# Kernel tuning notes

Measured on AMD Instinct MI355X. Metric: run time of the kernel, lower is better.

## Reference

```python
import jax, jax.numpy as jnp
import numpy as np

B, S, N_CATE, N_CONT = 32, 1024, 4, 4
HIDDEN, ATTN, VOCAB, EMB = 1024, 512, 1000, 128


def sinusoidal_pe(seq_len, d_model, base=10000.0):
    pos = jnp.arange(seq_len, dtype=jnp.float32)[:, None]            # [S,1]
    i = jnp.arange(d_model // 2, dtype=jnp.float32)[None, :]         # [1,D/2]
    ang = pos / jnp.power(base, 2.0 * i / d_model)                   # [S,D/2]
    pe = jnp.zeros((seq_len, d_model), dtype=jnp.float32)
    pe = pe.at[:, 0::2].set(jnp.sin(ang))
    pe = pe.at[:, 1::2].set(jnp.cos(ang))
    return pe


def setup_inputs() -> dict:
    key = jax.random.key(0)
    ks = jax.random.split(key, 20)
    s = 0.02
    inp = {
        "cate_x": jax.random.randint(ks[0], (B, S, N_CATE), 0, VOCAB, dtype=jnp.int64)
                  if jax.config.read("jax_enable_x64") else
                  jax.random.randint(ks[0], (B, S, N_CATE), 0, VOCAB, dtype=jnp.int32),
        "cont_x": jax.random.normal(ks[1], (B, S, N_CONT), dtype=jnp.float32),
        "mask": jnp.ones((B, S), dtype=bool),
        "targets": jax.random.uniform(ks[2], (B, S), dtype=jnp.float32),
        # EntireEmbedding params: 4 cate tables + cont linear + comb projection
        "E0": jax.random.normal(ks[3], (VOCAB, EMB), dtype=jnp.float32) * s,
        "E1": jax.random.normal(ks[4], (VOCAB, EMB), dtype=jnp.float32) * s,
        "E2": jax.random.normal(ks[5], (VOCAB, EMB), dtype=jnp.float32) * s,
        "E3": jax.random.normal(ks[6], (VOCAB, EMB), dtype=jnp.float32) * s,
        "Wc": jax.random.normal(ks[7], (N_CONT, N_CATE * EMB), dtype=jnp.float32) * s,
        "Wproj": jax.random.normal(ks[8], (2 * N_CATE * EMB, HIDDEN), dtype=jnp.float32) * s,
        # two-head attention linears (bias=False)
        "WQ1": jax.random.normal(ks[9], (HIDDEN, ATTN), dtype=jnp.float32) * s,
        "WK1": jax.random.normal(ks[10], (HIDDEN, ATTN), dtype=jnp.float32) * s,
        "WV1": jax.random.normal(ks[11], (HIDDEN, ATTN), dtype=jnp.float32) * s,
        "WQ2": jax.random.normal(ks[12], (HIDDEN, ATTN), dtype=jnp.float32) * s,
        "WK2": jax.random.normal(ks[13], (HIDDEN, ATTN), dtype=jnp.float32) * s,
        "WV2": jax.random.normal(ks[14], (HIDDEN, ATTN), dtype=jnp.float32) * s,
        "W0": jax.random.normal(ks[15], (2 * ATTN, HIDDEN), dtype=jnp.float32) * s,
        "Wf": jax.random.normal(ks[16], (HIDDEN, 1), dtype=jnp.float32) * s,
    }
    return inp


def _attend(x, WQ, WK, WV):
    Q = x @ WQ  # [B,S,A]
    K = x @ WK
    V = x @ WV
    scores = jnp.einsum("bqd,bkd->bqk", Q, K) / jnp.sqrt(jnp.float32(ATTN))
    # faithful to nn.Softmax(dim=1): normalize over the QUERY axis
    attn = jax.nn.softmax(scores, axis=1)
    return jnp.einsum("bqk,bkv->bqv", attn, V)


def reference(cate_x, cont_x, mask, targets, E0, E1, E2, E3, Wc, Wproj,
              WQ1, WK1, WV1, WQ2, WK2, WV2, W0, Wf):
    # EntireEmbedding: per-feature cate embeddings + cont projection -> comb proj
    cate_emb = jnp.concatenate(
        [E0[cate_x[..., 0]], E1[cate_x[..., 1]], E2[cate_x[..., 2]], E3[cate_x[..., 3]]],
        axis=-1)                                   # [B,S,512]
    cont_emb = cont_x @ Wc                          # [B,S,512]
    x = jnp.concatenate([cate_emb, cont_emb], axis=-1) @ Wproj  # [B,S,H]
    x = x + sinusoidal_pe(x.shape[1], HIDDEN)[None, :, :]
    z1 = _attend(x, WQ1, WK1, WV1)                  # [B,S,A]
    z2 = _attend(x, WQ2, WK2, WV2)                  # [B,S,A]
    z = jnp.concatenate([z1, z2], axis=-1) @ W0     # [B,S,H]
    out = jax.nn.sigmoid(z @ Wf)                    # FinalConnecting: Linear(H,1)+sigmoid
    return out.squeeze(-1)                          # [B,S]
```

## Files before the change

### kernel.cpp

```cpp
#include <hip/hip_runtime.h>
#include <hip/hip_bf16.h>
#include <math.h>

#define BB    32
#define SS    1024
#define HID   1024
#define AT    512
#define NVOC  1000
#define NT    (BB*SS)

typedef unsigned short u16;
typedef __attribute__((ext_vector_type(8))) short s16x8;
typedef __attribute__((ext_vector_type(4))) float f32x4;

__device__ __forceinline__ float bf2f(u16 u) {
    union { unsigned int i; float f; } x; x.i = ((unsigned int)u) << 16; return x.f;
}
__device__ __forceinline__ u16 f2bf(float f) {
    union { float f; unsigned int i; } u; u.f = f;
    unsigned int r = u.i + 0x7fffu + ((u.i >> 16) & 1u);
    return (u16)(r >> 16);
}
__device__ __forceinline__ float4 ld4(const float* p) { return *(const float4*)p; }
__device__ __forceinline__ float4 ld4bf(const u16* p) {
    ushort4 v = *(const ushort4*)p;
    return make_float4(bf2f(v.x), bf2f(v.y), bf2f(v.z), bf2f(v.w));
}

__device__ __forceinline__ void gld16(const u16* g, u16* l) {
    __builtin_amdgcn_global_load_lds(
        (const __attribute__((address_space(1))) unsigned int*)g,
        (__attribute__((address_space(3))) unsigned int*)l,
        16, 0, 0);
}

struct Ptrs4f { const float* p[4]; };

__device__ __forceinline__ float blockReduceSum(float x) {
    #pragma unroll
    for (int off = 32; off > 0; off >>= 1) x += __shfl_down(x, off, 64);
    __shared__ float tmp[4];
    int lane = threadIdx.x & 63, wid = threadIdx.x >> 6;
    if (lane == 0) tmp[wid] = x;
    __syncthreads();
    if (threadIdx.x == 0) x = tmp[0] + tmp[1] + tmp[2] + tmp[3];
    return x;
}
__device__ __forceinline__ float waveReduceSum(float x) {
    #pragma unroll
    for (int off = 32; off > 0; off >>= 1) x += __shfl_down(x, off, 64);
    return x;
}

__global__ void k_prep(Ptrs4f E, const float* __restrict__ Wproj,
                       u16* __restrict__ PE16, u16* __restrict__ E16o, u16* __restrict__ Wp16) {
    int blk = blockIdx.x, tid = threadIdx.x;
    if (blk < 2048) {
        int idx = blk*256 + tid;
        int s = idx >> 9, i = idx & 511;
        const float l2_10000 = 13.287712379549449f;
        float denom = exp2f((2.f * (float)i / 1024.f) * l2_10000);
        float ang = (float)s / denom;
        unsigned int pack = ((unsigned int)f2bf(cosf(ang)) << 16) | f2bf(sinf(ang));
        *(unsigned int*)(PE16 + (size_t)s*1024 + 2*i) = pack;
    } else if (blk < 4048) {
        int id2 = blk - 2048;
        int f = id2 / 500;
        int i = (id2 % 500)*256 + tid;
        E16o[(size_t)f*128000 + i] = f2bf(E.p[f][i]);
    } else {
        int i = (blk - 4048)*256 + tid;
        Wp16[i] = f2bf(Wproj[i]);
    }
}

__global__ void k_transp(Ptrs4f src, u16* __restrict__ dst, int R, int C) {
    const float* in = src.p[blockIdx.z];
    u16* out = dst + (size_t)blockIdx.z * R * C;
    int r0 = blockIdx.y*32, c0 = blockIdx.x*32;
    __shared__ float tt[32][33];
    tt[threadIdx.y][threadIdx.x] = in[(size_t)(r0 + threadIdx.y)*C + c0 + threadIdx.x];
    __syncthreads();
    out[(size_t)(c0 + threadIdx.y)*R + r0 + threadIdx.x] = f2bf(tt[threadIdx.x][threadIdx.y]);
}

__global__ void k_pre1(const float* __restrict__ W0, const float* __restrict__ Wf,
                       const float* __restrict__ Wc, const float* __restrict__ Wproj,
                       float* __restrict__ W0f, float* __restrict__ Wcp, float* __restrict__ CQ) {
    int blk = blockIdx.x, tid = threadIdx.x;
    if (blk < 1024) {
        const float* row = W0 + (size_t)blk*1024;
        float a = 0.f;
        for (int j = tid; j < 1024; j += 256) a += row[j] * Wf[j];
        a = blockReduceSum(a);
        if (tid == 0) W0f[blk] = a;
    } else if (blk < 1040) {
        int r = blk - 1024; int c = r >> 2, is = r & 3; int i = is*256 + tid;
        float a = 0.f;
        for (int j = 0; j < 512; ++j) a += Wc[c*512 + j] * Wproj[(size_t)(512 + j)*1024 + i];
        Wcp[c*1024 + i] = a;
    } else {
        int r = blk - 1040;
        CQ[r*256 + tid] = 0.f;
    }
}

__global__ void k_pre2(Ptrs4f W, const float* __restrict__ WV1, const float* __restrict__ WV2,
                       const float* __restrict__ W0f, const float* __restrict__ Wcp,
                       float* __restrict__ v, float* __restrict__ CQ) {
    int blk = blockIdx.x, tid = threadIdx.x;
    if (blk < 2048) {
        int h = blk >> 10, i = blk & 1023;
        const float* WV = h ? WV2 : WV1;
        const float* wf = W0f + h*512;
        float a = 0.f;
        for (int aa = tid; aa < 512; aa += 256) a += WV[(size_t)i*512 + aa] * wf[aa];
        a = blockReduceSum(a);
        if (tid == 0) v[h*1024 + i] = a;
    } else {
        int r = blk - 2048;
        int ns = r & 1, wc = (r >> 1) & 15, jc = r >> 5;
        int w = wc & 3, c = wc >> 2; int n = ns*256 + tid;
        const float* Ww = W.p[w];
        float a = 0.f;
        for (int j = jc*128; j < jc*128 + 128; ++j) a += Wcp[c*1024 + j] * Ww[(size_t)j*512 + n];
        atomicAdd(&CQ[(size_t)(w*4 + c)*512 + n], a);
    }
}

__device__ __forceinline__ void cstore(float* p, float v) { *p = v; }
__device__ __forceinline__ void cstore(u16* p, float v)   { *p = f2bf(v); }

template<typename CT, bool STATS, bool CTRANS>
__device__ __forceinline__ void mfma_gemm(const u16* __restrict__ A, const u16* __restrict__ B,
                                          CT* __restrict__ C, int M, int N, int K, float alpha,
                                          float* __restrict__ dcol, int m0, int n0) {
    __shared__ u16 As[128*64];
    __shared__ u16 Bs[128*64];
    const int tid = threadIdx.x;
    const int wave = tid >> 6, lane = tid & 63;
    const int quad = lane >> 4, l16 = lane & 15;
    const int wm = (wave >> 1)*64, wn = (wave & 1)*64;
    const int srow = lane >> 3;
    const int scol = ((lane & 7) ^ srow) * 8;
    f32x4 acc[4][4] = {};

    for (int k0 = 0; k0 < K; k0 += 64) {
        #pragma unroll
        for (int p = 0; p < 4; ++p) {
            int rb = wave*32 + p*8;
            gld16(A + (size_t)(m0 + rb + srow)*K + k0 + scol, As + rb*64);
            gld16(B + (size_t)(n0 + rb + srow)*K + k0 + scol, Bs + rb*64);
        }
        __syncthreads();
        #pragma unroll
        for (int kk = 0; kk < 2; ++kk) {
            s16x8 af[4], bf[4];
            #pragma unroll
            for (int i = 0; i < 4; ++i) {
                int row = wm + i*16 + l16;
                af[i] = *(const s16x8*)(As + row*64 + (((kk*4 + quad) ^ (row & 7)) * 8));
            }
            #pragma unroll
            for (int j = 0; j < 4; ++j) {
                int row = wn + j*16 + l16;
                bf[j] = *(const s16x8*)(Bs + row*64 + (((kk*4 + quad) ^ (row & 7)) * 8));
            }
            #pragma unroll
            for (int i = 0; i < 4; ++i)
                #pragma unroll
                for (int j = 0; j < 4; ++j)
                    acc[i][j] = __builtin_amdgcn_mfma_f32_16x16x32_bf16(af[i], bf[j], acc[i][j], 0, 0, 0);
        }
        __syncthreads();
    }
    if (STATS) {
        #pragma unroll
        for (int i = 0; i < 4; ++i)
            #pragma unroll
            for (int r = 0; r < 4; ++r) {
                int gm = m0 + wm + i*16 + quad*4 + r;
                u16 b0 = f2bf(acc[i][0][r] * alpha);
                u16 b1 = f2bf(acc[i][1][r] * alpha);
                u16 b2 = f2bf(acc[i][2][r] * alpha);
                u16 b3 = f2bf(acc[i][3][r] * alpha);
                acc[i][0][r] = bf2f(b0); acc[i][1][r] = bf2f(b1);
                acc[i][2][r] = bf2f(b2); acc[i][3][r] = bf2f(b3);
                unsigned int lo = (unsigned int)b0 | ((unsigned int)b1 << 16);
                unsigned int hi = (unsigned int)b2 | ((unsigned int)b3 << 16);
                *(uint2*)((u16*)C + (size_t)gm*N + n0 + wn + l16*4) = make_uint2(lo, hi);
            }
        #pragma unroll
        for (int j = 0; j < 4; ++j) {
            float sm = 0.f;
            #pragma unroll
            for (int i = 0; i < 4; ++i)
                #pragma unroll
                for (int r = 0; r < 4; ++r) sm += exp2f(acc[i][j][r]);
            sm += __shfl_xor(sm, 16, 64);
            sm += __shfl_xor(sm, 32, 64);
            if (quad == 0) atomicAdd(&dcol[n0 + wn + j*16 + l16], sm);
        }
    } else {
        #pragma unroll
        for (int i = 0; i < 4; ++i) {
            #pragma unroll
            for (int r = 0; r < 4; ++r) {
                int gm = m0 + wm + i*16 + quad*4 + r;
                if (gm < M) {
                    #pragma unroll
                    for (int j = 0; j < 4; ++j) {
                        int gn = n0 + wn + j*16 + l16;
                        if (CTRANS) cstore(C + (size_t)gn*M + gm, acc[i][j][r] * alpha);
                        else        cstore(C + (size_t)gm*N + gn, acc[i][j][r] * alpha);
                    }
                }
            }
        }
    }
}

__global__ __launch_bounds__(256) void k_pw_pre3(const u16* __restrict__ Wp16, const u16* __restrict__ Wt,
                                                 u16* __restrict__ PWT,
                                                 const float* __restrict__ Wproj, const float* __restrict__ v,
                                                 float* __restrict__ pv) {
    int blk = blockIdx.x;
    if (blk < 64) {
        int x = blk & 3, z = blk >> 2;
        int f = z >> 2, w = z & 3;
        mfma_gemm<u16,false,true>(Wp16 + (size_t)f*128*1024, Wt + (size_t)w*512*1024,
                                  PWT + (size_t)z*512*128, 128, 512, 1024, 1.f,
                                  nullptr, 0, x*128);
    } else {
        int b2 = blk - 64, tid = threadIdx.x;
        int i = b2 & 127, fh = b2 >> 7; int f = fh >> 1, h = fh & 1;
        const float* row = Wproj + (size_t)(f*128 + i)*1024;
        const float* vh = v + h*1024;
        float a = 0.f;
        for (int j = tid; j < 1024; j += 256) a += row[j] * vh[j];
        a = blockReduceSum(a);
        if (tid == 0) pv[(size_t)fh*128 + i] = a;
    }
}

__global__ __launch_bounds__(256) void k_g_TP(const u16* __restrict__ E16, const u16* __restrict__ PWT,
                                              const u16* __restrict__ PE16, const u16* __restrict__ Wt,
                                              u16* __restrict__ TQK16, u16* __restrict__ PEQ16) {
    int z = blockIdx.z;
    if (z < 16) {
        int f = z >> 2;
        mfma_gemm<u16,false,false>(E16 + (size_t)f*128000, PWT + (size_t)z*512*128,
                   TQK16 + (size_t)z*1000*512, 1000, 512, 128, 1.f, nullptr,
                   blockIdx.y*128, blockIdx.x*128);
    } else {
        int w = z - 16;
        mfma_gemm<u16,false,false>(PE16, Wt + (size_t)w*512*1024, PEQ16 + (size_t)w*1024*512,
                   1024, 512, 1024, 1.f, nullptr, blockIdx.y*128, blockIdx.x*128);
    }
}

__global__ __launch_bounds__(256) void k_g_S(const u16* __restrict__ Q, const u16* __restrict__ K,
                                             u16* __restrict__ Sb, float alpha,
                                             float* __restrict__ d, int b0) {
    size_t b = blockIdx.z;
    int bx = (blockIdx.x % 4)*2 + (blockIdx.y % 2);
    int by = (blockIdx.x / 4)*4 + (blockIdx.y / 2);
    mfma_gemm<u16,true,false>(Q + b*SS*AT, K + b*SS*AT, Sb + b*SS*SS, 1024, 1024, 512, alpha,
                        d + ((size_t)(b0 + b) << 10), by*128, bx*128);
}

__global__ void k_dots(const u16* __restrict__ E16, const u16* __restrict__ PE16,
                       const float* __restrict__ Wcp, const float* __restrict__ v,
                       const float* __restrict__ pv,
                       float* __restrict__ Ut, float* __restrict__ pu, float* __restrict__ cu) {
    int id = blockIdx.x;
    if (id < 2000) {
        int wave = threadIdx.x >> 6, lane = threadIdx.x & 63;
        int d = id*4 + wave;
        int f = d / 2000, h = (d / 1000) & 1, r = d % 1000;
        unsigned int e2 = *(const unsigned int*)(E16 + ((size_t)f*1000 + r)*128 + lane*2);
        const float* pvp = pv + (size_t)(f*2 + h)*128 + lane*2;
        float a = bf2f((u16)(e2 & 0xffff)) * pvp[0] + bf2f((u16)(e2 >> 16)) * pvp[1];
        a = waveReduceSum(a);
        if (lane == 0) Ut[(size_t)(f*2 + h)*1000 + r] = a;
    } else if (id < 4048) {
        int tq = id - 2000; int h = tq >> 10, s = tq & 1023;
        float4 a = ld4bf(PE16 + (size_t)s*1024 + threadIdx.x*4);
        float4 b = ld4(v + h*1024 + threadIdx.x*4);
        float p = a.x*b.x + a.y*b.y + a.z*b.z + a.w*b.w;
        p = blockReduceSum(p);
        if (threadIdx.x == 0) pu[h*1024 + s] = p;
    } else {
        int tq = id - 4048; int h = tq >> 2, c = tq & 3;
        float4 a = ld4(Wcp + c*1024 + threadIdx.x*4);
        float4 b = ld4(v + h*1024 + threadIdx.x*4);
        float p = a.x*b.x + a.y*b.y + a.z*b.z + a.w*b.w;
        p = blockReduceSum(p);
        if (threadIdx.x == 0) cu[h*4 + c] = p;
    }
}

__device__ __forceinline__ void unpack8(uint4 v, float* x) {
    x[0] = bf2f((u16)(v.x & 0xffff)); x[1] = bf2f((u16)(v.x >> 16));
    x[2] = bf2f((u16)(v.y & 0xffff)); x[3] = bf2f((u16)(v.y >> 16));
    x[4] = bf2f((u16)(v.z & 0xffff)); x[5] = bf2f((u16)(v.z >> 16));
    x[6] = bf2f((u16)(v.w & 0xffff)); x[7] = bf2f((u16)(v.w >> 16));
}

__global__ void k_gather(const int* __restrict__ cate, const float* __restrict__ cont,
                         const u16* __restrict__ TQK, const float* __restrict__ CQ,
                         const u16* __restrict__ PEQ, const float* __restrict__ Ut,
                         const float* __restrict__ cu, const float* __restrict__ pu,
                         u16* __restrict__ Qh, u16* __restrict__ Kh,
                         float* __restrict__ u, float* __restrict__ dzero, int h) {
    int tid = threadIdx.x;
    if (blockIdx.x < 128) dzero[blockIdx.x*256 + tid] = 0.f;
    size_t t = (size_t)blockIdx.x*2 + (tid >> 7);
    int r = tid & 127;
    int s = (int)(t & 1023);
    int4 cc = *(const int4*)(cate + t*4);
    float4 cv = ld4(cont + t*4);
    int e = r >> 6;
    int w = 2*h + e;
    int n = (r & 63)*8;
    const u16* t0 = TQK + ((size_t)(0*4  + w)*1000 + cc.x)*512 + n;
    const u16* t1 = TQK + ((size_t)(1*4  + w)*1000 + cc.y)*512 + n;
    const u16* t2 = TQK + ((size_t)(2*4  + w)*1000 + cc.z)*512 + n;
    const u16* t3 = TQK + ((size_t)(3*4  + w)*1000 + cc.w)*512 + n;
    const u16* pq = PEQ + ((size_t)w*1024 + s)*512 + n;
    const float* cq = CQ + (size_t)w*2048 + n;
    float a0[8], a1[8], a2[8], a3[8], ap[8];
    unpack8(*(const uint4*)t0, a0); unpack8(*(const uint4*)t1, a1);
    unpack8(*(const uint4*)t2, a2); unpack8(*(const uint4*)t3, a3);
    unpack8(*(const uint4*)pq, ap);
    unsigned int pack[4];
    #pragma unroll
    for (int jp = 0; jp < 4; ++jp) {
        float x0, x1;
        #pragma unroll
        for (int half = 0; half < 2; ++half) {
            int j = jp*2 + half;
            float x = a0[j] + a1[j] + a2[j] + a3[j] + ap[j]
                    + cv.x*cq[j] + cv.y*cq[512+j] + cv.z*cq[1024+j] + cv.w*cq[1536+j];
            if (half == 0) x0 = x; else x1 = x;
        }
        pack[jp] = ((unsigned int)f2bf(x1) << 16) | f2bf(x0);
    }
    u16* op = (e ? Kh : Qh) + t*512 + n;
    *(uint4*)op = make_uint4(pack[0], pack[1], pack[2], pack[3]);
    if (r == 0) {
        float uu = pu[h*1024 + s]
                 + Ut[(0*2 + h)*1000 + cc.x] + Ut[(1*2 + h)*1000 + cc.y]
                 + Ut[(2*2 + h)*1000 + cc.z] + Ut[(3*2 + h)*1000 + cc.w]
                 + cv.x*cu[h*4+0] + cv.y*cu[h*4+1] + cv.z*cu[h*4+2] + cv.w*cu[h*4+3];
        u[(size_t)h*NT + t] = uu;
    }
}

__global__ void k_wexp(const float* __restrict__ d, const float* __restrict__ u,
                       float* __restrict__ wexp, int b0) {
    int idx = b0*1024 + blockIdx.x*256 + threadIdx.x;
    int b = idx >> 10, k = idx & 1023;
    int q = (k & ~63) | (((k & 15) << 2) | ((k & 63) >> 4));
    wexp[((size_t)b << 10) + q] = u[idx] / d[idx];
}

__global__ void k_logit(const u16* __restrict__ Sb, const float* __restrict__ wexp,
                        float* __restrict__ logits, int b0, int init) {
    int wave = threadIdx.x >> 6, lane = threadIdx.x & 63;
    size_t tl = (size_t)blockIdx.x*4 + wave;
    size_t tabs = (size_t)b0*1024 + tl;
    int b = (int)(tabs >> 10);
    const u16* row = Sb + tl*1024;
    const float* wb = wexp + ((size_t)b << 10);
    float acc = 0.f;
    #pragma unroll
    for (int half = 0; half < 2; ++half) {
        int k = lane*8 + half*512;
        float4 s0 = ld4bf(row + k), s1 = ld4bf(row + k + 4);
        float4 w0 = ld4(wb + k),    w1 = ld4(wb + k + 4);
        acc += exp2f(s0.x)*w0.x + exp2f(s0.y)*w0.y + exp2f(s0.z)*w0.z + exp2f(s0.w)*w0.w
             + exp2f(s1.x)*w1.x + exp2f(s1.y)*w1.y + exp2f(s1.z)*w1.z + exp2f(s1.w)*w1.w;
    }
    acc = waveReduceSum(acc);
    if (lane == 0) { if (init) logits[tabs] = acc; else logits[tabs] += acc; }
}

__global__ void k_final(const float* __restrict__ logits, float* __restrict__ out) {
    int t = blockIdx.x*256 + threadIdx.x;
    float x = logits[t];
    out[t] = 1.f / (1.f + expf(-x));
}

extern "C" void kernel_launch(void* const* d_in, const int* in_sizes, int n_in,
                              void* d_out, int out_size, void* d_ws, size_t ws_size,
                              hipStream_t stream) {
    const int*   cate = (const int*)d_in[0];
    const float* cont = (const float*)d_in[1];
    Ptrs4f E; E.p[0] = (const float*)d_in[4]; E.p[1] = (const float*)d_in[5];
              E.p[2] = (const float*)d_in[6]; E.p[3] = (const float*)d_in[7];
    const float* Wc    = (const float*)d_in[8];
    const float* Wproj = (const float*)d_in[9];
    Ptrs4f W; W.p[0] = (const float*)d_in[10];
              W.p[1] = (const float*)d_in[11];
              W.p[2] = (const float*)d_in[13];
              W.p[3] = (const float*)d_in[14];
    const float* WV1 = (const float*)d_in[12];
    const float* WV2 = (const float*)d_in[15];
    const float* W0  = (const float*)d_in[16];
    const float* Wf  = (const float*)d_in[17];

    char* base = (char*)d_ws;
    size_t off = 0;
    auto alloc = [&](size_t bytes) { void* p = base + off; off += (bytes + 255) & ~(size_t)255; return p; };
    u16*   PE16  = (u16*)  alloc(1048576ull*2);
    u16*   E16   = (u16*)  alloc(4ull*1000*128*2);
    u16*   Wt    = (u16*)  alloc(4ull*512*1024*2);
    u16*   Wp16  = (u16*)  alloc(512ull*1024*2);
    u16*   PWT   = (u16*)  alloc(16ull*512*128*2);
    u16*   TQK16 = (u16*)  alloc(16ull*1000*512*2);
    u16*   PEQ16 = (u16*)  alloc(4ull*1024*512*2);
    float* Wcp   = (float*)alloc(4*1024*4);
    float* W0f   = (float*)alloc(1024*4);
    float* vv    = (float*)alloc(2*1024*4);
    float* CQ    = (float*)alloc(16*512*4);
    float* pvb   = (float*)alloc(8*128*4);
    float* Ut    = (float*)alloc(8*1000*4);
    float* cu    = (float*)alloc(8*4);
    float* pu    = (float*)alloc(2*1024*4);
    float* ubuf  = (float*)alloc(2ull*NT*4);
    u16*   Qh    = (u16*)  alloc((size_t)NT*512*2);
    u16*   Kh    = (u16*)  alloc((size_t)NT*512*2);
    float* dbuf  = (float*)alloc(32ull*1024*4);
    float* wbuf  = (float*)alloc(32*1024*4);
    float* logits= (float*)alloc((size_t)NT*4);
    size_t sChunkBytes = (size_t)SS*SS*2;
    size_t remain = (ws_size > off) ? (ws_size - off) : 0;
    int NB = (int)(remain / sChunkBytes);
    if (NB > 32) NB = 32;
    if (NB < 1) NB = 1;
    u16* Sbuf = (u16*)(base + off);

    const float alpha = 0.06375954951107036f;

    k_prep<<<6096, 256, 0, stream>>>(E, Wproj, PE16, E16, Wp16);
    k_transp<<<dim3(16, 32, 4), dim3(32, 32), 0, stream>>>(W, Wt, 1024, 512);
    k_pre1<<<1072, 256, 0, stream>>>(W0, Wf, Wc, Wproj, W0f, Wcp, CQ);
    k_pre2<<<2304, 256, 0, stream>>>(W, WV1, WV2, W0f, Wcp, vv, CQ);
    k_pw_pre3<<<1088, 256, 0, stream>>>(Wp16, Wt, PWT, Wproj, vv, pvb);
    k_g_TP<<<dim3(4, 8, 20), 256, 0, stream>>>(E16, PWT, PE16, Wt, TQK16, PEQ16);
    k_dots<<<4056, 256, 0, stream>>>(E16, PE16, Wcp, vv, pvb, Ut, pu, cu);

    for (int h = 0; h < 2; ++h) {
        k_gather<<<NT/2, 256, 0, stream>>>(cate, cont, TQK16, CQ, PEQ16, Ut, cu, pu, Qh, Kh, ubuf, dbuf, h);
        for (int b0 = 0; b0 < 32; b0 += NB) {
            int nb = (32 - b0 < NB) ? (32 - b0) : NB;
            k_g_S<<<dim3(8, 8, nb), 256, 0, stream>>>(Qh + (size_t)b0*SS*AT, Kh + (size_t)b0*SS*AT, Sbuf, alpha, dbuf, b0);
            k_wexp<<<nb*4, 256, 0, stream>>>(dbuf, ubuf + (size_t)h*NT, wbuf, b0);
            k_logit<<<nb*256, 256, 0, stream>>>(Sbuf, wbuf, logits, b0, h == 0 ? 1 : 0);
        }
    }
    k_final<<<128, 256, 0, stream>>>(logits, (float*)d_out);
}
```

Baseline: 413.5 us.

## Replace atomic column-sum stats with per-tile max/sum partials and combine kernel

The score GEMM epilogue now computes a column-wise max and a max-shifted exp-sum per 128-row tile, merges the wave partials in shared memory, and writes them to per-tile buffers instead of atomically adding raw exp sums. A new combine kernel reduces the eight row-tile partials into a stable denominator, and the zeroing of the old denominator buffer in the gather kernel is removed. This removes global atomics and adds numerical stability, at the cost of extra exp work, a block-wide barrier in the epilogue and larger partial buffers. Launch bounds for the score kernel also now request an occupancy of 6.

After: 393.1 us. -4.9%, faster.

```diff
diff --git a/kernel.cpp b/kernel.cpp
--- a/kernel.cpp
+++ b/kernel.cpp
@@ -134,7 +134,8 @@
 template<typename CT, bool STATS, bool CTRANS>
 __device__ __forceinline__ void mfma_gemm(const u16* __restrict__ A, const u16* __restrict__ B,
                                           CT* __restrict__ C, int M, int N, int K, float alpha,
-                                          float* __restrict__ dcol, int m0, int n0) {
+                                          float* __restrict__ Pm, float* __restrict__ Pd,
+                                          int m0, int n0) {
     __shared__ u16 As[128*64];
     __shared__ u16 Bs[128*64];
     const int tid = threadIdx.x;
@@ -190,16 +191,36 @@
                 unsigned int hi = (unsigned int)b2 | ((unsigned int)b3 << 16);
                 *(uint2*)((u16*)C + (size_t)gm*N + n0 + wn + l16*4) = make_uint2(lo, hi);
             }
+        __shared__ float sMax[4][64];
+        __shared__ float sSum[4][64];
         #pragma unroll
         for (int j = 0; j < 4; ++j) {
-            float sm = 0.f;
+            float mx = -3.4e38f;
             #pragma unroll
             for (int i = 0; i < 4; ++i)
                 #pragma unroll
-                for (int r = 0; r < 4; ++r) sm += exp2f(acc[i][j][r]);
+                for (int r = 0; r < 4; ++r) mx = fmaxf(mx, acc[i][j][r]);
+            mx = fmaxf(mx, __shfl_xor(mx, 16, 64));
+            mx = fmaxf(mx, __shfl_xor(mx, 32, 64));
+            float sm = 0.f;
+            #pragma unroll
+            for (int i = 0; i < 4; ++i)
+                #pragma unroll
+                for (int r = 0; r < 4; ++r) sm += exp2f(acc[i][j][r] - mx);
             sm += __shfl_xor(sm, 16, 64);
             sm += __shfl_xor(sm, 32, 64);
-            if (quad == 0) atomicAdd(&dcol[n0 + wn + j*16 + l16], sm);
+            if (quad == 0) { sMax[wave][j*16 + l16] = mx; sSum[wave][j*16 + l16] = sm; }
+        }
+        __syncthreads();
+        if (tid < 128) {
+            int c = tid;
+            int w0 = (c < 64) ? 0 : 1, ci = c & 63;
+            float m0v = sMax[w0][ci],     s0 = sSum[w0][ci];
+            float m1v = sMax[w0 + 2][ci], s1 = sSum[w0 + 2][ci];
+            float mm = fmaxf(m0v, m1v);
+            float ss = s0 * exp2f(m0v - mm) + s1 * exp2f(m1v - mm);
+            Pm[n0 + c] = mm;
+            Pd[n0 + c] = ss;
         }
     } else {
         #pragma unroll
@@ -230,7 +251,7 @@
         int f = z >> 2, w = z & 3;
         mfma_gemm<u16,false,true>(Wp16 + (size_t)f*128*1024, Wt + (size_t)w*512*1024,
                                   PWT + (size_t)z*512*128, 128, 512, 1024, 1.f,
-                                  nullptr, 0, x*128);
+                                  nullptr, nullptr, 0, x*128);
     } else {
         int b2 = blk - 64, tid = threadIdx.x;
         int i = b2 & 127, fh = b2 >> 7; int f = fh >> 1, h = fh & 1;
@@ -250,23 +271,24 @@
     if (z < 16) {
         int f = z >> 2;
         mfma_gemm<u16,false,false>(E16 + (size_t)f*128000, PWT + (size_t)z*512*128,
-                   TQK16 + (size_t)z*1000*512, 1000, 512, 128, 1.f, nullptr,
+                   TQK16 + (size_t)z*1000*512, 1000, 512, 128, 1.f, nullptr, nullptr,
                    blockIdx.y*128, blockIdx.x*128);
     } else {
         int w = z - 16;
         mfma_gemm<u16,false,false>(PE16, Wt + (size_t)w*512*1024, PEQ16 + (size_t)w*1024*512,
-                   1024, 512, 1024, 1.f, nullptr, blockIdx.y*128, blockIdx.x*128);
-    }
-}
-
-__global__ __launch_bounds__(256) void k_g_S(const u16* __restrict__ Q, const u16* __restrict__ K,
+                   1024, 512, 1024, 1.f, nullptr, nullptr, blockIdx.y*128, blockIdx.x*128);
+    }
+}
+
+__global__ __launch_bounds__(256, 6) void k_g_S(const u16* __restrict__ Q, const u16* __restrict__ K,
                                              u16* __restrict__ Sb, float alpha,
-                                             float* __restrict__ d, int b0) {
+                                             float* __restrict__ Pm, float* __restrict__ Pd, int b0) {
     size_t b = blockIdx.z;
     int bx = (blockIdx.x % 4)*2 + (blockIdx.y % 2);
     int by = (blockIdx.x / 4)*4 + (blockIdx.y / 2);
+    size_t po = ((b0 + b)*8 + by)*1024;
     mfma_gemm<u16,true,false>(Q + b*SS*AT, K + b*SS*AT, Sb + b*SS*SS, 1024, 1024, 512, alpha,
-                        d + ((size_t)(b0 + b) << 10), by*128, bx*128);
+                        Pm + po, Pd + po, by*128, bx*128);
 }
 
 __global__ void k_dots(const u16* __restrict__ E16, const u16* __restrict__ PE16,
@@ -312,9 +334,8 @@
                          const u16* __restrict__ PEQ, const float* __restrict__ Ut,
                          const float* __restrict__ cu, const float* __restrict__ pu,
                          u16* __restrict__ Qh, u16* __restrict__ Kh,
-                         float* __restrict__ u, float* __restrict__ dzero, int h) {
+                         float* __restrict__ u, int h) {
     int tid = threadIdx.x;
-    if (blockIdx.x < 128) dzero[blockIdx.x*256 + tid] = 0.f;
     size_t t = (size_t)blockIdx.x*2 + (tid >> 7);
     int r = tid & 127;
     int s = (int)(t & 1023);
@@ -357,12 +378,19 @@
     }
 }
 
-__global__ void k_wexp(const float* __restrict__ d, const float* __restrict__ u,
-                       float* __restrict__ wexp, int b0) {
+__global__ void k_stats_combine(const float* __restrict__ Pm, const float* __restrict__ Pd,
+                                const float* __restrict__ u, float* __restrict__ wexp, int b0) {
     int idx = b0*1024 + blockIdx.x*256 + threadIdx.x;
     int b = idx >> 10, k = idx & 1023;
+    float mx = -3.4e38f;
+    #pragma unroll
+    for (int mt = 0; mt < 8; ++mt) mx = fmaxf(mx, Pm[((size_t)b*8 + mt)*1024 + k]);
+    float dd = 0.f;
+    #pragma unroll
+    for (int mt = 0; mt < 8; ++mt) dd += Pd[((size_t)b*8 + mt)*1024 + k]
+                                       * exp2f(Pm[((size_t)b*8 + mt)*1024 + k] - mx);
     int q = (k & ~63) | (((k & 15) << 2) | ((k & 63) >> 4));
-    wexp[((size_t)b << 10) + q] = u[idx] / d[idx];
+    wexp[((size_t)b << 10) + q] = u[idx] / dd * exp2f(-mx);
 }
 
 __global__ void k_logit(const u16* __restrict__ Sb, const float* __restrict__ wexp,
@@ -431,7 +459,8 @@
     float* ubuf  = (float*)alloc(2ull*NT*4);
     u16*   Qh    = (u16*)  alloc((size_t)NT*512*2);
     u16*   Kh    = (u16*)  alloc((size_t)NT*512*2);
-    float* dbuf  = (float*)alloc(32ull*1024*4);
+    float* Pm    = (float*)alloc(32ull*8*1024*4);
+    float* Pd    = (float*)alloc(32ull*8*1024*4);
     float* wbuf  = (float*)alloc(32*1024*4);
     float* logits= (float*)alloc((size_t)NT*4);
     size_t sChunkBytes = (size_t)SS*SS*2;
@@ -452,11 +481,11 @@
     k_dots<<<4056, 256, 0, stream>>>(E16, PE16, Wcp, vv, pvb, Ut, pu, cu);
 
     for (int h = 0; h < 2; ++h) {
-        k_gather<<<NT/2, 256, 0, stream>>>(cate, cont, TQK16, CQ, PEQ16, Ut, cu, pu, Qh, Kh, ubuf, dbuf, h);
+        k_gather<<<NT/2, 256, 0, stream>>>(cate, cont, TQK16, CQ, PEQ16, Ut, cu, pu, Qh, Kh, ubuf, h);
         for (int b0 = 0; b0 < 32; b0 += NB) {
             int nb = (32 - b0 < NB) ? (32 - b0) : NB;
-            k_g_S<<<dim3(8, 8, nb), 256, 0, stream>>>(Qh + (size_t)b0*SS*AT, Kh + (size_t)b0*SS*AT, Sbuf, alpha, dbuf, b0);
-            k_wexp<<<nb*4, 256, 0, stream>>>(dbuf, ubuf + (size_t)h*NT, wbuf, b0);
+            k_g_S<<<dim3(8, 8, nb), 256, 0, stream>>>(Qh + (size_t)b0*SS*AT, Kh + (size_t)b0*SS*AT, Sbuf, alpha, Pm, Pd, b0);
+            k_stats_combine<<<nb*4, 256, 0, stream>>>(Pm, Pd, ubuf + (size_t)h*NT, wbuf, b0);
             k_logit<<<nb*256, 256, 0, stream>>>(Sbuf, wbuf, logits, b0, h == 0 ? 1 : 0);
         }
     }
```
